# Optimization experiments

Hardware: AMD Instinct MI355X
Metric: run time of the kernel (lower is better)

Reference implementation:

```python
import jax, jax.numpy as jnp
import numpy as np

B, S, DIN = 16, 960, 7
HID, HEADS, LAYERS = 512, 8, 4
PERIODS = (24, 48, 96)
OUT_LEN = 96
HEAD_DIM = HID // HEADS
FFN = 4 * HID


def setup_inputs() -> dict:
    key = jax.random.key(0)
    ks = jax.random.split(key, 20)
    sc = 0.02
    return {
        "x": jax.random.normal(ks[0], (B, S, DIN), dtype=jnp.float32),
        "input_proj_w": jax.random.normal(ks[1], (HID, DIN), dtype=jnp.float32) * sc,
        "input_proj_b": jnp.zeros((HID,), dtype=jnp.float32),
        "in_proj_w": jax.random.normal(ks[2], (LAYERS, 3 * HID, HID), dtype=jnp.float32) * sc,
        "in_proj_b": jnp.zeros((LAYERS, 3 * HID), dtype=jnp.float32),
        "out_proj_w": jax.random.normal(ks[3], (LAYERS, HID, HID), dtype=jnp.float32) * sc,
        "out_proj_b": jnp.zeros((LAYERS, HID), dtype=jnp.float32),
        "ffn_w1": jax.random.normal(ks[4], (LAYERS, FFN, HID), dtype=jnp.float32) * sc,
        "ffn_b1": jnp.zeros((LAYERS, FFN), dtype=jnp.float32),
        "ffn_w2": jax.random.normal(ks[5], (LAYERS, HID, FFN), dtype=jnp.float32) * sc,
        "ffn_b2": jnp.zeros((LAYERS, HID), dtype=jnp.float32),
        "ln1_w": jnp.ones((LAYERS, HID), dtype=jnp.float32),
        "ln1_b": jnp.zeros((LAYERS, HID), dtype=jnp.float32),
        "ln2_w": jnp.ones((LAYERS, HID), dtype=jnp.float32),
        "ln2_b": jnp.zeros((LAYERS, HID), dtype=jnp.float32),
        "output_proj_w": jax.random.normal(ks[6], (1, HID), dtype=jnp.float32) * sc,
        "output_proj_b": jnp.zeros((1,), dtype=jnp.float32),
    }


def _layer_norm(x, w, b, eps=1e-5):
    mu = jnp.mean(x, axis=-1, keepdims=True)
    var = jnp.mean(jnp.square(x - mu), axis=-1, keepdims=True)
    return (x - mu) * jax.lax.rsqrt(var + eps) * w + b


def _mha(x, wqkv, bqkv, wo, bo):
    # x: [N, P, H]; self-attention, PyTorch nn.MultiheadAttention math (eval mode)
    N, P, _ = x.shape
    qkv = x @ wqkv.T + bqkv                      # [N, P, 3H]
    q, k, v = jnp.split(qkv, 3, axis=-1)
    q = q.reshape(N, P, HEADS, HEAD_DIM)
    k = k.reshape(N, P, HEADS, HEAD_DIM)
    v = v.reshape(N, P, HEADS, HEAD_DIM)
    scores = jnp.einsum("nqhd,nkhd->nhqk", q, k) / jnp.sqrt(jnp.float32(HEAD_DIM))
    attn = jax.nn.softmax(scores, axis=-1)
    out = jnp.einsum("nhqk,nkhd->nqhd", attn, v).reshape(N, P, HID)
    return out @ wo.T + bo


def _times_block(x, period, wqkv, bqkv, wo, bo, w1, b1, w2, b2, g1, be1, g2, be2):
    # x: [B, S, H], S % period == 0. Batch all period slices together
    # (replaces the original Python loop over num_periods).
    Bc, Sc, H = x.shape
    xb = x.reshape(Bc * (Sc // period), period, H)
    attn = _mha(xb, wqkv, bqkv, wo, bo)
    xb = _layer_norm(xb + attn, g1, be1)
    ffn = jax.nn.gelu(xb @ w1.T + b1, approximate=False) @ w2.T + b2
    xb = _layer_norm(xb + ffn, g2, be2)
    return xb.reshape(Bc, Sc, H)


def reference(x, input_proj_w, input_proj_b, in_proj_w, in_proj_b, out_proj_w,
              out_proj_b, ffn_w1, ffn_b1, ffn_w2, ffn_b2, ln1_w, ln1_b,
              ln2_w, ln2_b, output_proj_w, output_proj_b):
    h = x @ input_proj_w.T + input_proj_b        # [B, S, H]
    branches = []
    for period in PERIODS:
        ph = h
        for l in range(LAYERS):
            ph = _times_block(ph, period,
                              in_proj_w[l], in_proj_b[l], out_proj_w[l], out_proj_b[l],
                              ffn_w1[l], ffn_b1[l], ffn_w2[l], ffn_b2[l],
                              ln1_w[l], ln1_b[l], ln2_w[l], ln2_b[l])
        branches.append(ph)
    h = jnp.mean(jnp.stack(branches, axis=0), axis=0)     # [B, S, H]
    out = h @ output_proj_w.T + output_proj_b             # [B, S, 1]
    # AdaptiveAvgPool1d(OUT_LEN) with S % OUT_LEN == 0 -> uniform block mean
    out = out.reshape(B, OUT_LEN, S // OUT_LEN, 1).mean(axis=2)  # [B, OUT_LEN, 1]
    return out
```

## Files before the change

### kernel.cpp

```cpp
#include <hip/hip_runtime.h>
#include <hip/hip_bf16.h>

typedef __bf16 bf16;
typedef __attribute__((ext_vector_type(8))) __bf16 bf16x8;
typedef __attribute__((ext_vector_type(4))) __bf16 bf16x4;
typedef __attribute__((ext_vector_type(4))) float f32x4;

#define TOKENS 15360
#define HID    512
#define FFN_D  2048
#define QKV_D  1536

__device__ __forceinline__ float gelu_erf(float x) {
  const float z = fabsf(x) * 0.70710678118654752f;
#if __has_builtin(__builtin_amdgcn_rcpf)
  const float t = __builtin_amdgcn_rcpf(fmaf(0.3275911f, z, 1.f));
#else
  const float t = 1.f / fmaf(0.3275911f, z, 1.f);
#endif
  float p = fmaf(1.061405429f, t, -1.453152027f);
  p = fmaf(p, t, 1.421413741f);
  p = fmaf(p, t, -0.284496736f);
  p = fmaf(p, t, 0.254829592f);
  p *= t;
  const float e  = __expf(-z * z);
  const float er = fmaf(-p, e, 1.f);
  return 0.5f * x * (1.f + copysignf(er, x));
}

__global__ __launch_bounds__(256) void cvt_kernel(const float* __restrict__ src,
                                                  bf16* __restrict__ dst, int n4) {
  const int i = (blockIdx.x * 256 + threadIdx.x);
  if (i >= n4) return;
  const float4 v = ((const float4*)src)[i];
  bf16x4 d = {(bf16)v.x, (bf16)v.y, (bf16)v.z, (bf16)v.w};
  *(bf16x4*)(dst + (size_t)i * 4) = d;
}

__global__ __launch_bounds__(256) void cvt_w2_kernel(const float* __restrict__ src,
                                                     bf16* __restrict__ dst, int n4) {
  const int i = (blockIdx.x * 256 + threadIdx.x);
  if (i >= n4) return;
  const int f  = i * 4;
  const int ln = f >> 11;
  const int c2 = f & 2047;
  const int h  = c2 >> 10;
  const int c  = c2 & 1023;
  const int l  = ln >> 9;
  const int n  = ln & 511;
  const float4 v = ((const float4*)src)[i];
  bf16x4 d = {(bf16)v.x, (bf16)v.y, (bf16)v.z, (bf16)v.w};
  *(bf16x4*)(dst + ((((size_t)(l * 2 + h) * 512 + n) << 10) + c)) = d;
}

#define EPI_BIAS_BF16     0
#define EPI_BIAS_RES_BF16 1
#define EPI_BIAS_GELU     2
#define EPI_RES_BF16      3

template <int EPI>
__global__ __launch_bounds__(256) void gemm_bt(
    const bf16* __restrict__ A, const bf16* __restrict__ W,
    const float* __restrict__ bias, const bf16* __restrict__ R,
    bf16* __restrict__ out, int M, int N, int K) {
  __shared__ __align__(16) bf16 As[2 * 128 * 64];
  __shared__ __align__(16) bf16 Bs[2 * 128 * 64];

  const int tid  = threadIdx.x;
  const int lane = tid & 63;
  const int wv   = tid >> 6;
  const int li   = lane & 15;
  const int qd   = lane >> 4;
  const int mw   = (wv & 1) << 6;
  const int nw   = (wv >> 1) << 6;

  const int NB  = gridDim.x;
  const int nwg = NB * gridDim.y;
  int lid = blockIdx.y * NB + blockIdx.x;
  if ((nwg & 7) == 0) lid = (lid & 7) * (nwg >> 3) + (lid >> 3);
  const int n0 = (lid % NB) << 7;
  const int m0 = (lid / NB) << 7;

  f32x4 acc[4][4];
#pragma unroll
  for (int i = 0; i < 4; ++i)
#pragma unroll
    for (int j = 0; j < 4; ++j) acc[i][j] = (f32x4){0.f, 0.f, 0.f, 0.f};

  const bf16* pa[4];
  const bf16* pb[4];
  int off[4];
#pragma unroll
  for (int it = 0; it < 4; ++it) {
    const int fc   = it * 256 + tid;
    const int r    = fc >> 3;
    const int c    = fc & 7;
    const int koff = (c ^ (r & 7)) << 3;
    pa[it]  = A + (size_t)(m0 + r) * K + koff;
    pb[it]  = W + (size_t)(n0 + r) * K + koff;
    off[it] = (it * 256 + (tid & 192)) * 8;
  }

  auto stage = [&](int buf) {
#pragma unroll
    for (int it = 0; it < 4; ++it) {
      __builtin_amdgcn_global_load_lds(
          (const __attribute__((address_space(1))) unsigned int*)pa[it],
          (__attribute__((address_space(3))) unsigned int*)(As + buf * 8192 + off[it]),
          16, 0, 0);
      pa[it] += 64;
    }
#pragma unroll
    for (int it = 0; it < 4; ++it) {
      __builtin_amdgcn_global_load_lds(
          (const __attribute__((address_space(1))) unsigned int*)pb[it],
          (__attribute__((address_space(3))) unsigned int*)(Bs + buf * 8192 + off[it]),
          16, 0, 0);
      pb[it] += 64;
    }
  };

  auto compute = [&](int buf) {
    const bf16* Ab = As + buf * 8192;
    const bf16* Bb = Bs + buf * 8192;
#pragma unroll
    for (int ks = 0; ks < 2; ++ks) {
      const int ck = (ks << 2) + qd;
      bf16x8 af[4], bfv[4];
#pragma unroll
      for (int i = 0; i < 4; ++i) {
        const int mr = mw + i * 16 + li;
        af[i] = *(const bf16x8*)(Ab + mr * 64 + ((ck ^ (li & 7)) << 3));
      }
#pragma unroll
      for (int j = 0; j < 4; ++j) {
        const int nr = nw + j * 16 + li;
        bfv[j] = *(const bf16x8*)(Bb + nr * 64 + ((ck ^ (li & 7)) << 3));
      }
#pragma unroll
      for (int i = 0; i < 4; ++i)
#pragma unroll
        for (int j = 0; j < 4; ++j)
          acc[i][j] = __builtin_amdgcn_mfma_f32_16x16x32_bf16(af[i], bfv[j],
                                                              acc[i][j], 0, 0, 0);
    }
  };

  stage(0);
  int cur = 0;
  for (int k0 = 0; k0 < K - 64; k0 += 64) {
    stage(cur ^ 1);
    asm volatile("s_waitcnt vmcnt(8)" ::: "memory");
    __builtin_amdgcn_s_barrier();
    asm volatile("" ::: "memory");
    compute(cur);
    asm volatile("" ::: "memory");
    __builtin_amdgcn_s_barrier();
    asm volatile("" ::: "memory");
    cur ^= 1;
  }
  asm volatile("s_waitcnt vmcnt(0)" ::: "memory");
  __builtin_amdgcn_s_barrier();
  asm volatile("" ::: "memory");
  compute(cur);

#pragma unroll
  for (int i = 0; i < 4; ++i) {
    const int mrow = m0 + mw + i * 16 + qd * 4;
#pragma unroll
    for (int j = 0; j < 4; ++j) {
      const int ncol = n0 + nw + j * 16 + li;
      float bv = 0.f;
      if (EPI != EPI_RES_BF16) bv = bias[ncol];
#pragma unroll
      for (int r = 0; r < 4; ++r) {
        const size_t off2 = (size_t)(mrow + r) * N + ncol;
        float v = acc[i][j][r] + bv;
        if (EPI == EPI_BIAS_RES_BF16 || EPI == EPI_RES_BF16) v += (float)R[off2];
        out[off2] = (EPI == EPI_BIAS_GELU) ? (bf16)gelu_erf(v) : (bf16)v;
      }
    }
  }
}

template <int P>
__global__ __launch_bounds__(256) void attn_kernel(const bf16* __restrict__ qkv,
                                                   bf16* __restrict__ out) {
  constexpr int PP   = ((P + 15) / 16) * 16;
  constexpr int PK   = ((PP + 31) / 32) * 32;
  constexpr int MT   = PP / 16;
  constexpr int SSTR = PP + 2;
  constexpr int VSTR = PK + 8;
  constexpr int PSTR = PK + 8;
  constexpr int G    = (P * 8 <= 256) ? 8 : ((P * 4 <= 256) ? 4 : 2);

  __shared__ __align__(16) bf16 QK[2 * PP * 64];
  __shared__ __align__(16) bf16 Vt[64 * VSTR];
  __shared__ __align__(16) float Sm[PP * SSTR];
  __shared__ float rsum[PP];

  bf16* Qs = QK;
  bf16* Ks = QK + PP * 64;
  bf16* Ps = QK;

  const int tid  = threadIdx.x;
  const int lane = tid & 63;
  const int wv   = tid >> 6;
  const int li   = lane & 15;
  const int qd   = lane >> 4;
  const int n    = blockIdx.x >> 3;
  const int h    = blockIdx.x & 7;
  const bf16* base = qkv + (size_t)n * P * QKV_D + h * 64;

  for (int t = tid; t < P * 8; t += 256) {
    const int r = t >> 3, c = t & 7;
    const bf16x8 qv = *(const bf16x8*)(base + (size_t)r * QKV_D + c * 8);
    const bf16x8 kv = *(const bf16x8*)(base + (size_t)r * QKV_D + 512 + c * 8);
    *(bf16x8*)(Qs + r * 64 + ((c ^ (r & 7)) * 8)) = qv;
    *(bf16x8*)(Ks + r * 64 + ((c ^ (r & 7)) * 8)) = kv;
  }
  for (int t = tid; t < P * 8; t += 256) {
    const int j = t % P, dc = t / P;
    const bf16x8 vv = *(const bf16x8*)(base + (size_t)j * QKV_D + 1024 + dc * 8);
#pragma unroll
    for (int u = 0; u < 8; ++u) Vt[(dc * 8 + u) * VSTR + j] = vv[u];
  }
  if constexpr (PK > P) {
    for (int t = tid; t < 64 * (PK - P); t += 256) {
      const int d = t / (PK - P), j = P + t % (PK - P);
      Vt[d * VSTR + j] = (bf16)0.f;
    }
  }
  __syncthreads();

  for (int t = wv; t < MT * MT; t += 4) {
    const int ti = t / MT, tj = t % MT;
    f32x4 acc = (f32x4){0.f, 0.f, 0.f, 0.f};
#pragma unroll
    for (int ks = 0; ks < 2; ++ks) {
      const int ck = ks * 4 + qd;
      const int ar = ti * 16 + li;
      const int br = tj * 16 + li;
      const bf16x8 af = *(const bf16x8*)(Qs + ar * 64 + ((ck ^ (ar & 7)) * 8));
      const bf16x8 bv = *(const bf16x8*)(Ks + br * 64 + ((ck ^ (br & 7)) * 8));
      acc = __builtin_amdgcn_mfma_f32_16x16x32_bf16(af, bv, acc, 0, 0, 0);
    }
#pragma unroll
    for (int r = 0; r < 4; ++r)
      Sm[(ti * 16 + qd * 4 + r) * SSTR + tj * 16 + li] = acc[r];
  }
  __syncthreads();

  if (tid < P * G) {
    const int row = tid / G, g = tid % G;
    const float* srow = Sm + row * SSTR;
    bf16* prow = Ps + row * PSTR;
    float mx = -1e30f;
    for (int j = g; j < P; j += G) mx = fmaxf(mx, srow[j]);
#pragma unroll
    for (int m = G >> 1; m; m >>= 1) mx = fmaxf(mx, __shfl_xor(mx, m, 64));
    mx *= 0.125f;
    float sum = 0.f;
    for (int j = g; j < P; j += G) {
      const float e = __expf(srow[j] * 0.125f - mx);
      sum += e;
      prow[j] = (bf16)e;
    }
#pragma unroll
    for (int m = G >> 1; m; m >>= 1) sum += __shfl_xor(sum, m, 64);
    for (int j = P + g; j < PK; j += G) prow[j] = (bf16)0.f;
    if (g == 0) rsum[row] = 1.f / sum;
  }
  __syncthreads();

  for (int t = wv; t < MT * 4; t += 4) {
    const int ti = t >> 2, td = t & 3;
    f32x4 acc = (f32x4){0.f, 0.f, 0.f, 0.f};
#pragma unroll
    for (int ks = 0; ks < PK / 32; ++ks) {
      const int ck = ks * 4 + qd;
      const bf16x8 af = *(const bf16x8*)(Ps + (ti * 16 + li) * PSTR + ck * 8);
      const bf16x8 bv = *(const bf16x8*)(Vt + (td * 16 + li) * VSTR + ck * 8);
      acc = __builtin_amdgcn_mfma_f32_16x16x32_bf16(af, bv, acc, 0, 0, 0);
    }
#pragma unroll
    for (int r = 0; r < 4; ++r) {
      const int row = ti * 16 + qd * 4 + r;
      if (row < P)
        out[(size_t)(n * P + row) * HID + h * 64 + td * 16 + li] =
            (bf16)(acc[r] * rsum[row]);
    }
  }
}

__global__ __launch_bounds__(256) void ln_kernel(const bf16* __restrict__ Y,
                                                 const float* __restrict__ w,
                                                 const float* __restrict__ b,
                                                 bf16* __restrict__ X) {
  const int row  = blockIdx.x * 4 + (threadIdx.x >> 6);
  const int lane = threadIdx.x & 63;
  const bf16x8 yv = *(const bf16x8*)(Y + (size_t)row * HID + 8 * lane);
  float y[8];
#pragma unroll
  for (int u = 0; u < 8; ++u) y[u] = (float)yv[u];
  float s = 0.f, s2 = 0.f;
#pragma unroll
  for (int u = 0; u < 8; ++u) { s += y[u]; s2 += y[u] * y[u]; }
#pragma unroll
  for (int off = 32; off > 0; off >>= 1) {
    s  += __shfl_xor(s, off, 64);
    s2 += __shfl_xor(s2, off, 64);
  }
  const float mean = s * (1.f / 512.f);
  const float var  = s2 * (1.f / 512.f) - mean * mean;
  const float rstd = rsqrtf(var + 1e-5f);
  const float4 w0 = ((const float4*)w)[2 * lane];
  const float4 w1 = ((const float4*)w)[2 * lane + 1];
  const float4 b0 = ((const float4*)b)[2 * lane];
  const float4 b1 = ((const float4*)b)[2 * lane + 1];
  const float wr[8] = {w0.x, w0.y, w0.z, w0.w, w1.x, w1.y, w1.z, w1.w};
  const float br[8] = {b0.x, b0.y, b0.z, b0.w, b1.x, b1.y, b1.z, b1.w};
  bf16x8 o;
#pragma unroll
  for (int u = 0; u < 8; ++u) o[u] = (bf16)((y[u] - mean) * rstd * wr[u] + br[u]);
  *(bf16x8*)(X + (size_t)row * HID + 8 * lane) = o;
}

__global__ __launch_bounds__(256) void inproj_kernel(const float* __restrict__ x,
                                                     const float* __restrict__ w,
                                                     const float* __restrict__ b,
                                                     bf16* __restrict__ h,
                                                     int nbr) {
  const int idx = blockIdx.x * 256 + threadIdx.x;
  const int r = idx >> 9, o = idx & 511;
  float s = b[o];
#pragma unroll
  for (int k = 0; k < 7; ++k) s += x[r * 7 + k] * w[o * 7 + k];
  const bf16 bv = (bf16)s;
  for (int q = 0; q < nbr; ++q) h[idx + (size_t)q * TOKENS * HID] = bv;
}

__global__ __launch_bounds__(256) void outdot_kernel(const bf16* __restrict__ X,
                                                     const float* __restrict__ w,
                                                     float* __restrict__ acc,
                                                     int first) {
  const int row  = blockIdx.x * 4 + (threadIdx.x >> 6);
  const int lane = threadIdx.x & 63;
  const bf16* xr = X + (size_t)row * HID;
  const bf16x8 xa = *(const bf16x8*)(xr + 8 * lane);
  const float4 wa = ((const float4*)w)[2 * lane];
  const float4 wb = ((const float4*)w)[2 * lane + 1];
  float s = (float)xa[0] * wa.x + (float)xa[1] * wa.y + (float)xa[2] * wa.z +
            (float)xa[3] * wa.w + (float)xa[4] * wb.x + (float)xa[5] * wb.y +
            (float)xa[6] * wb.z + (float)xa[7] * wb.w;
#pragma unroll
  for (int off = 32; off > 0; off >>= 1) s += __shfl_xor(s, off, 64);
  if (lane == 0) acc[row] = first ? s : (acc[row] + s);
}

__global__ __launch_bounds__(256) void pool_kernel(const float* __restrict__ acc,
                                                   const float* __restrict__ ob,
                                                   float* __restrict__ out) {
  const int idx = blockIdx.x * 256 + threadIdx.x;
  if (idx >= 16 * 96) return;
  const int bb = idx / 96, o = idx % 96;
  float s = 0.f;
#pragma unroll
  for (int j = 0; j < 10; ++j) s += acc[bb * 960 + o * 10 + j];
  out[idx] = s * (1.f / 30.f) + ob[0];
}

extern "C" void kernel_launch(void* const* d_in, const int* in_sizes, int n_in,
                              void* d_out, int out_size, void* d_ws,
                              size_t ws_size, hipStream_t stream) {
  const float* x          = (const float*)d_in[0];
  const float* ip_w       = (const float*)d_in[1];
  const float* ip_b       = (const float*)d_in[2];
  const float* in_proj_w  = (const float*)d_in[3];
  const float* in_proj_b  = (const float*)d_in[4];
  const float* out_proj_w = (const float*)d_in[5];
  const float* out_proj_b = (const float*)d_in[6];
  const float* ffn_w1     = (const float*)d_in[7];
  const float* ffn_b1     = (const float*)d_in[8];
  const float* ffn_w2     = (const float*)d_in[9];
  const float* ffn_b2     = (const float*)d_in[10];
  const float* ln1_w      = (const float*)d_in[11];
  const float* ln1_b      = (const float*)d_in[12];
  const float* ln2_w      = (const float*)d_in[13];
  const float* ln2_b      = (const float*)d_in[14];
  const float* op_w       = (const float*)d_in[15];
  const float* op_b       = (const float*)d_in[16];

  char* p = (char*)d_ws;
  bf16* Wq = (bf16*)p; p += (size_t)4 * QKV_D * HID * 2;
  bf16* Wo = (bf16*)p; p += (size_t)4 * HID * HID * 2;
  bf16* W1 = (bf16*)p; p += (size_t)4 * FFN_D * HID * 2;
  bf16* W2 = (bf16*)p; p += (size_t)4 * HID * FFN_D * 2;
  float* ACC = (float*)p; p += (size_t)TOKENS * 4;
  const size_t remain = ws_size - (size_t)(p - (char*)d_ws);

  const size_t T3 = 3 * (size_t)TOKENS;
  const size_t need_unsplit = T3 * HID * 2 + T3 * (size_t)FFN_D * 2 + T3 * HID * 2;
  const size_t need_split   = T3 * HID * 2 + T3 * (size_t)FFN_D * 2;
  const size_t need_seq     = (size_t)TOKENS * HID * 2 + (size_t)TOKENS * FFN_D * 2;
  const bool unsplit = remain >= need_unsplit;
  const bool batched = remain >= need_split;
  if (!batched && remain < need_seq) return;

  {
    const int nq = 4 * QKV_D * HID / 4, no = 4 * HID * HID / 4,
              n1 = 4 * FFN_D * HID / 4, n2 = 4 * HID * FFN_D / 4;
    cvt_kernel<<<(nq + 255) / 256, 256, 0, stream>>>(in_proj_w, Wq, nq);
    cvt_kernel<<<(no + 255) / 256, 256, 0, stream>>>(out_proj_w, Wo, no);
    cvt_kernel<<<(n1 + 255) / 256, 256, 0, stream>>>(ffn_w1, W1, n1);
    if (unsplit)
      cvt_kernel<<<(n2 + 255) / 256, 256, 0, stream>>>(ffn_w2, W2, n2);
    else
      cvt_w2_kernel<<<(n2 + 255) / 256, 256, 0, stream>>>(ffn_w2, W2, n2);
  }

  static const int periods[3] = {24, 48, 96};
  auto launch_attn = [&](int P, const bf16* q, bf16* o) {
    const int nblk = (TOKENS / P) * 8;
    if (P == 24)      attn_kernel<24><<<nblk, 256, 0, stream>>>(q, o);
    else if (P == 48) attn_kernel<48><<<nblk, 256, 0, stream>>>(q, o);
    else              attn_kernel<96><<<nblk, 256, 0, stream>>>(q, o);
  };

  auto run_layer = [&](int l, int M, int qkvM, bf16* X, bf16* QKV, bf16* ATT,
                       bf16* YB, bf16* H, bool all_br, int br, bool unspl) {
    const int MB = M / 128;
    gemm_bt<EPI_BIAS_BF16><<<dim3(QKV_D / 128, qkvM / 128), 256, 0, stream>>>(
        X, Wq + (size_t)l * QKV_D * HID, in_proj_b + l * QKV_D, nullptr,
        QKV, qkvM, QKV_D, HID);
    if (all_br) {
      for (int b2 = 0; b2 < 3; ++b2) {
        const bf16* q = QKV + (qkvM == M ? (size_t)b2 * TOKENS * QKV_D : 0);
        launch_attn(periods[b2], q, ATT + (size_t)b2 * TOKENS * HID);
      }
    } else {
      launch_attn(periods[br], QKV, ATT);
    }
    gemm_bt<EPI_BIAS_RES_BF16><<<dim3(HID / 128, MB), 256, 0, stream>>>(
        ATT, Wo + (size_t)l * HID * HID, out_proj_b + l * HID, X, YB,
        M, HID, HID);
    ln_kernel<<<M / 4, 256, 0, stream>>>(YB, ln1_w + l * HID, ln1_b + l * HID, X);
    if (unspl) {
      gemm_bt<EPI_BIAS_GELU><<<dim3(FFN_D / 128, MB), 256, 0, stream>>>(
          X, W1 + (size_t)l * FFN_D * HID, ffn_b1 + l * FFN_D, nullptr,
          H, M, FFN_D, HID);
      gemm_bt<EPI_BIAS_RES_BF16><<<dim3(HID / 128, MB), 256, 0, stream>>>(
          H, W2 + (size_t)l * HID * FFN_D, ffn_b2 + l * HID, X, YB,
          M, HID, FFN_D);
    } else {
      gemm_bt<EPI_BIAS_GELU><<<dim3(1024 / 128, MB), 256, 0, stream>>>(
          X, W1 + (size_t)l * FFN_D * HID, ffn_b1 + l * FFN_D, nullptr,
          H, M, 1024, HID);
      gemm_bt<EPI_BIAS_RES_BF16><<<dim3(HID / 128, MB), 256, 0, stream>>>(
          H, W2 + (size_t)(l * 2 + 0) * HID * 1024, ffn_b2 + l * HID, X, YB,
          M, HID, 1024);
      gemm_bt<EPI_BIAS_GELU><<<dim3(1024 / 128, MB), 256, 0, stream>>>(
          X, W1 + (size_t)l * FFN_D * HID + (size_t)1024 * HID,
          ffn_b1 + l * FFN_D + 1024, nullptr, H, M, 1024, HID);
      gemm_bt<EPI_RES_BF16><<<dim3(HID / 128, MB), 256, 0, stream>>>(
          H, W2 + (size_t)(l * 2 + 1) * HID * 1024, nullptr, YB, YB,
          M, HID, 1024);
    }
    ln_kernel<<<M / 4, 256, 0, stream>>>(YB, ln2_w + l * HID, ln2_b + l * HID, X);
  };

  if (batched) {
    bf16* X   = (bf16*)p; p += T3 * HID * 2;
    bf16* BUF = (bf16*)p; p += T3 * (size_t)FFN_D * 2;
    bf16* QKV = BUF;
    bf16* ATT = BUF + T3 * QKV_D;
    bf16* H, * YB;
    if (unsplit) {
      H  = BUF;
      YB = (bf16*)p;
    } else {
      H  = BUF;
      YB = BUF + T3 * 1024;
    }
    const int M = (int)T3;

    inproj_kernel<<<TOKENS * HID / 256, 256, 0, stream>>>(x, ip_w, ip_b, X, 3);
    for (int l = 0; l < 4; ++l)
      run_layer(l, M, l == 0 ? TOKENS : M, X, QKV, ATT, YB, H, true, 0, unsplit);
    for (int br = 0; br < 3; ++br)
      outdot_kernel<<<TOKENS / 4, 256, 0, stream>>>(
          X + (size_t)br * TOKENS * HID, op_w, ACC, br == 0);
  } else {
    bf16* X   = (bf16*)p; p += (size_t)TOKENS * HID * 2;
    bf16* SCR = (bf16*)p; p += (size_t)TOKENS * FFN_D * 2;
    bf16* QKV = SCR;
    bf16* ATT = SCR + (size_t)TOKENS * QKV_D;
    bf16* H   = SCR;
    bf16* YB  = SCR + (size_t)TOKENS * 1024;
    const int M = TOKENS;

    for (int br = 0; br < 3; ++br) {
      inproj_kernel<<<TOKENS * HID / 256, 256, 0, stream>>>(x, ip_w, ip_b, X, 1);
      for (int l = 0; l < 4; ++l)
        run_layer(l, M, M, X, QKV, ATT, YB, H, false, br, false);
      outdot_kernel<<<TOKENS / 4, 256, 0, stream>>>(X, op_w, ACC, br == 0);
    }
  }
  pool_kernel<<<6, 256, 0, stream>>>(ACC, op_b, (float*)d_out);
}
```

Measured before the change: 2.214 ms.

## Use 512-thread GEMM blocks with a four-stage LDS prefetch pipeline

The bf16 GEMM moves from 4 to 8 waves per 128x128 tile, so each wave computes a 64x32 sub-tile. The LDS ring grows from double to quadruple buffering, with three K-tiles kept in flight and graded vmcnt waits for the tail. The aim is to hide global-load latency and add latency tolerance through more waves per block. In exchange, LDS use per block doubles to 128 KB, which limits how many blocks fit per CU, and each wave issues more LDS fragment reads relative to its MFMA work.

```diff
diff --git a/kernel.cpp b/kernel.cpp
--- a/kernel.cpp
+++ b/kernel.cpp
@@ -59,20 +59,20 @@
 #define EPI_RES_BF16      3
 
 template <int EPI>
-__global__ __launch_bounds__(256) void gemm_bt(
+__global__ __launch_bounds__(512) void gemm_bt(
     const bf16* __restrict__ A, const bf16* __restrict__ W,
     const float* __restrict__ bias, const bf16* __restrict__ R,
     bf16* __restrict__ out, int M, int N, int K) {
-  __shared__ __align__(16) bf16 As[2 * 128 * 64];
-  __shared__ __align__(16) bf16 Bs[2 * 128 * 64];
+  __shared__ __align__(16) bf16 As[4 * 128 * 64];
+  __shared__ __align__(16) bf16 Bs[4 * 128 * 64];
 
   const int tid  = threadIdx.x;
   const int lane = tid & 63;
   const int wv   = tid >> 6;
   const int li   = lane & 15;
   const int qd   = lane >> 4;
-  const int mw   = (wv & 1) << 6;
-  const int nw   = (wv >> 1) << 6;
+  const int mw   = (wv >> 2) << 6;
+  const int nw   = (wv & 3) << 5;
 
   const int NB  = gridDim.x;
   const int nwg = NB * gridDim.y;
@@ -81,29 +81,29 @@
   const int n0 = (lid % NB) << 7;
   const int m0 = (lid / NB) << 7;
 
-  f32x4 acc[4][4];
+  f32x4 acc[4][2];
 #pragma unroll
   for (int i = 0; i < 4; ++i)
 #pragma unroll
-    for (int j = 0; j < 4; ++j) acc[i][j] = (f32x4){0.f, 0.f, 0.f, 0.f};
-
-  const bf16* pa[4];
-  const bf16* pb[4];
-  int off[4];
-#pragma unroll
-  for (int it = 0; it < 4; ++it) {
-    const int fc   = it * 256 + tid;
-    const int r    = fc >> 3;
-    const int c    = fc & 7;
+    for (int j = 0; j < 2; ++j) acc[i][j] = (f32x4){0.f, 0.f, 0.f, 0.f};
+
+  const bf16* pa[2];
+  const bf16* pb[2];
+  int off[2];
+#pragma unroll
+  for (int it = 0; it < 2; ++it) {
+    const int q    = it * 512 + tid;
+    const int r    = q >> 3;
+    const int c    = q & 7;
     const int koff = (c ^ (r & 7)) << 3;
     pa[it]  = A + (size_t)(m0 + r) * K + koff;
     pb[it]  = W + (size_t)(n0 + r) * K + koff;
-    off[it] = (it * 256 + (tid & 192)) * 8;
+    off[it] = (it * 512 + (tid & 448)) * 8;
   }
 
   auto stage = [&](int buf) {
 #pragma unroll
-    for (int it = 0; it < 4; ++it) {
+    for (int it = 0; it < 2; ++it) {
       __builtin_amdgcn_global_load_lds(
           (const __attribute__((address_space(1))) unsigned int*)pa[it],
           (__attribute__((address_space(3))) unsigned int*)(As + buf * 8192 + off[it]),
@@ -111,7 +111,7 @@
       pa[it] += 64;
     }
 #pragma unroll
-    for (int it = 0; it < 4; ++it) {
+    for (int it = 0; it < 2; ++it) {
       __builtin_amdgcn_global_load_lds(
           (const __attribute__((address_space(1))) unsigned int*)pb[it],
           (__attribute__((address_space(3))) unsigned int*)(Bs + buf * 8192 + off[it]),
@@ -126,49 +126,47 @@
 #pragma unroll
     for (int ks = 0; ks < 2; ++ks) {
       const int ck = (ks << 2) + qd;
-      bf16x8 af[4], bfv[4];
-#pragma unroll
-      for (int i = 0; i < 4; ++i) {
-        const int mr = mw + i * 16 + li;
-        af[i] = *(const bf16x8*)(Ab + mr * 64 + ((ck ^ (li & 7)) << 3));
-      }
-#pragma unroll
-      for (int j = 0; j < 4; ++j) {
-        const int nr = nw + j * 16 + li;
-        bfv[j] = *(const bf16x8*)(Bb + nr * 64 + ((ck ^ (li & 7)) << 3));
-      }
+      const int sl = (ck ^ (li & 7)) << 3;
+      bf16x8 af[4], bfv[2];
 #pragma unroll
       for (int i = 0; i < 4; ++i)
-#pragma unroll
-        for (int j = 0; j < 4; ++j)
+        af[i] = *(const bf16x8*)(Ab + (mw + i * 16 + li) * 64 + sl);
+#pragma unroll
+      for (int j = 0; j < 2; ++j)
+        bfv[j] = *(const bf16x8*)(Bb + (nw + j * 16 + li) * 64 + sl);
+#pragma unroll
+      for (int i = 0; i < 4; ++i)
+#pragma unroll
+        for (int j = 0; j < 2; ++j)
           acc[i][j] = __builtin_amdgcn_mfma_f32_16x16x32_bf16(af[i], bfv[j],
                                                               acc[i][j], 0, 0, 0);
     }
   };
 
+  const int nt = K >> 6;
   stage(0);
-  int cur = 0;
-  for (int k0 = 0; k0 < K - 64; k0 += 64) {
-    stage(cur ^ 1);
-    asm volatile("s_waitcnt vmcnt(8)" ::: "memory");
+  stage(1);
+  stage(2);
+  for (int t = 0; t < nt; ++t) {
+    if (t + 3 < nt) stage((t + 3) & 3);
+    const int rem = nt - 1 - t;
+    if (rem >= 3)      asm volatile("s_waitcnt vmcnt(12)" ::: "memory");
+    else if (rem == 2) asm volatile("s_waitcnt vmcnt(8)"  ::: "memory");
+    else if (rem == 1) asm volatile("s_waitcnt vmcnt(4)"  ::: "memory");
+    else               asm volatile("s_waitcnt vmcnt(0)"  ::: "memory");
     __builtin_amdgcn_s_barrier();
     asm volatile("" ::: "memory");
-    compute(cur);
+    compute(t & 3);
     asm volatile("" ::: "memory");
     __builtin_amdgcn_s_barrier();
     asm volatile("" ::: "memory");
-    cur ^= 1;
-  }
-  asm volatile("s_waitcnt vmcnt(0)" ::: "memory");
-  __builtin_amdgcn_s_barrier();
-  asm volatile("" ::: "memory");
-  compute(cur);
+  }
 
 #pragma unroll
   for (int i = 0; i < 4; ++i) {
     const int mrow = m0 + mw + i * 16 + qd * 4;
 #pragma unroll
-    for (int j = 0; j < 4; ++j) {
+    for (int j = 0; j < 2; ++j) {
       const int ncol = n0 + nw + j * 16 + li;
       float bv = 0.f;
       if (EPI != EPI_RES_BF16) bv = bias[ncol];
@@ -430,7 +428,7 @@
   auto run_layer = [&](int l, int M, int qkvM, bf16* X, bf16* QKV, bf16* ATT,
                        bf16* YB, bf16* H, bool all_br, int br, bool unspl) {
     const int MB = M / 128;
-    gemm_bt<EPI_BIAS_BF16><<<dim3(QKV_D / 128, qkvM / 128), 256, 0, stream>>>(
+    gemm_bt<EPI_BIAS_BF16><<<dim3(QKV_D / 128, qkvM / 128), 512, 0, stream>>>(
         X, Wq + (size_t)l * QKV_D * HID, in_proj_b + l * QKV_D, nullptr,
         QKV, qkvM, QKV_D, HID);
     if (all_br) {
@@ -441,28 +439,28 @@
     } else {
       launch_attn(periods[br], QKV, ATT);
     }
-    gemm_bt<EPI_BIAS_RES_BF16><<<dim3(HID / 128, MB), 256, 0, stream>>>(
+    gemm_bt<EPI_BIAS_RES_BF16><<<dim3(HID / 128, MB), 512, 0, stream>>>(
         ATT, Wo + (size_t)l * HID * HID, out_proj_b + l * HID, X, YB,
         M, HID, HID);
     ln_kernel<<<M / 4, 256, 0, stream>>>(YB, ln1_w + l * HID, ln1_b + l * HID, X);
     if (unspl) {
-      gemm_bt<EPI_BIAS_GELU><<<dim3(FFN_D / 128, MB), 256, 0, stream>>>(
+      gemm_bt<EPI_BIAS_GELU><<<dim3(FFN_D / 128, MB), 512, 0, stream>>>(
           X, W1 + (size_t)l * FFN_D * HID, ffn_b1 + l * FFN_D, nullptr,
           H, M, FFN_D, HID);
-      gemm_bt<EPI_BIAS_RES_BF16><<<dim3(HID / 128, MB), 256, 0, stream>>>(
+      gemm_bt<EPI_BIAS_RES_BF16><<<dim3(HID / 128, MB), 512, 0, stream>>>(
           H, W2 + (size_t)l * HID * FFN_D, ffn_b2 + l * HID, X, YB,
           M, HID, FFN_D);
     } else {
-      gemm_bt<EPI_BIAS_GELU><<<dim3(1024 / 128, MB), 256, 0, stream>>>(
+      gemm_bt<EPI_BIAS_GELU><<<dim3(1024 / 128, MB), 512, 0, stream>>>(
           X, W1 + (size_t)l * FFN_D * HID, ffn_b1 + l * FFN_D, nullptr,
           H, M, 1024, HID);
-      gemm_bt<EPI_BIAS_RES_BF16><<<dim3(HID / 128, MB), 256, 0, stream>>>(
+      gemm_bt<EPI_BIAS_RES_BF16><<<dim3(HID / 128, MB), 512, 0, stream>>>(
           H, W2 + (size_t)(l * 2 + 0) * HID * 1024, ffn_b2 + l * HID, X, YB,
           M, HID, 1024);
-      gemm_bt<EPI_BIAS_GELU><<<dim3(1024 / 128, MB), 256, 0, stream>>>(
+      gemm_bt<EPI_BIAS_GELU><<<dim3(1024 / 128, MB), 512, 0, stream>>>(
           X, W1 + (size_t)l * FFN_D * HID + (size_t)1024 * HID,
           ffn_b1 + l * FFN_D + 1024, nullptr, H, M, 1024, HID);
-      gemm_bt<EPI_RES_BF16><<<dim3(HID / 128, MB), 256, 0, stream>>>(
+      gemm_bt<EPI_RES_BF16><<<dim3(HID / 128, MB), 512, 0, stream>>>(
           H, W2 + (size_t)(l * 2 + 1) * HID * 1024, nullptr, YB, YB,
           M, HID, 1024);
     }
```

New measurement: 2.741 ms. 23.8% more time.
